# Optimization experiments

Hardware: AMD Instinct MI355X
Metric: run time of the kernel (lower is better)

## Reference

```python
import jax, jax.numpy as jnp
import numpy as np

BIGNET_DIM = 1024
N_LAYERS = 18   # 6 blocks * 3 QLoRALinear
N_LN = 5
GROUPS = 64     # 1024 / group_size(16)
GS = 16
RANK = 32
BATCH = 16384
EPS = 1e-5


def dequant(qw, scale):
    # qw: [O, G, gs] int 0..15, scale: [O, G] per-group max-abs norm
    w = (qw.astype(jnp.float32) / 15.0 * 2.0 - 1.0) * scale[..., None]
    return w.reshape(qw.shape[0], -1)  # [O, I]


def qlora_linear(x, qw, scale, b, a_w, b_w):
    w = dequant(qw, scale)                      # [O, I]
    base = x @ w.T + b                          # [N, O]
    lora = (x @ a_w.T) @ b_w.T                  # [N, r] @ [r, O]
    return base + lora


def layernorm(h, g, b):
    mu = h.mean(-1, keepdims=True)
    var = jnp.mean((h - mu) ** 2, -1, keepdims=True)
    return (h - mu) * jax.lax.rsqrt(var + EPS) * g + b


def setup_inputs() -> dict:
    key = jax.random.key(0)
    ks = jax.random.split(key, 8)
    x = jax.random.normal(ks[0], (BATCH, BIGNET_DIM), jnp.float32)
    qw = jax.random.randint(ks[1], (N_LAYERS, BIGNET_DIM, GROUPS, GS), 0, 16, jnp.int32)
    scale = jax.random.uniform(ks[2], (N_LAYERS, BIGNET_DIM, GROUPS), jnp.float32) * 0.05
    bias = jax.random.normal(ks[3], (N_LAYERS, BIGNET_DIM), jnp.float32) * 0.02
    la = jax.random.normal(ks[4], (N_LAYERS, RANK, BIGNET_DIM), jnp.float32) * (2.0 / BIGNET_DIM) ** 0.5
    # note: torch zero-inits lora_b; use small random values so the LoRA path is testable
    lb = jax.random.normal(ks[5], (N_LAYERS, BIGNET_DIM, RANK), jnp.float32) * 0.01
    ln_w = jnp.ones((N_LN, BIGNET_DIM), jnp.float32)
    ln_b = jnp.zeros((N_LN, BIGNET_DIM), jnp.float32)
    return {"x": x, "scale": scale, "bias": bias, "la": la, "lb": lb,
            "ln_w": ln_w, "ln_b": ln_b, "qw": qw}


def reference(x, scale, bias, la, lb, ln_w, ln_b, qw):
    h = x
    li = 0
    for blk in range(6):
        r = h
        for j in range(3):
            h = qlora_linear(h, qw[li], scale[li], bias[li], la[li], lb[li])
            li += 1
            if j < 2:
                h = jax.nn.relu(h)
        h = h + r
        if blk < 5:
            h = layernorm(h, ln_w[blk], ln_b[blk])
    return h
```

## Files before the change

### kernel.cpp

```cpp
#include <hip/hip_runtime.h>

typedef unsigned short UST;
typedef __attribute__((ext_vector_type(8))) __bf16 bf16x8;
typedef __attribute__((ext_vector_type(4))) float f32x4;

__device__ __forceinline__ float bf2f(UST u) {
    union { unsigned int i; float f; } v; v.i = ((unsigned int)u) << 16; return v.f;
}
__device__ __forceinline__ UST f2bf(float f) {
    union { float f; unsigned int i; } v; v.f = f;
    return (UST)((v.i + 0x7fffu + ((v.i >> 16) & 1u)) >> 16);
}

__device__ __forceinline__ void gl2lds16(const UST* g, UST* l) {
    __builtin_amdgcn_global_load_lds(
        (const __attribute__((address_space(1))) unsigned int*)g,
        (__attribute__((address_space(3))) unsigned int*)l, 16, 0, 0);
}

__global__ __launch_bounds__(256) void prep_w(
    const int* __restrict__ qw, const float* __restrict__ scale,
    const float* __restrict__ la, const float* __restrict__ lb,
    UST* __restrict__ wp)
{
    int l = blockIdx.x, ot = blockIdx.y, it = blockIdx.z;
    __shared__ float la_s[32 * 128];
    __shared__ float lb_s[128 * 32];
    const float* laL = la + (size_t)l * 32 * 1024;
    const float* lbL = lb + (size_t)l * 1024 * 32;
    int t = threadIdx.x;
    for (int e = t; e < 32 * 128; e += 256) {
        int r = e >> 7, i = e & 127;
        la_s[e] = laL[r * 1024 + it * 128 + i];
    }
    for (int e = t; e < 128 * 32; e += 256)
        lb_s[e] = lbL[(size_t)ot * 128 * 32 + e];
    __syncthreads();

    int o0 = (t >> 4) * 8;
    int i0 = (t & 15) * 8;
    float acc[8][8];
    #pragma unroll
    for (int a = 0; a < 8; a++)
        #pragma unroll
        for (int c = 0; c < 8; c++) acc[a][c] = 0.f;
    for (int r = 0; r < 32; ++r) {
        float bv[8], av[8];
        #pragma unroll
        for (int j = 0; j < 8; j++) bv[j] = lb_s[(o0 + j) * 32 + r];
        #pragma unroll
        for (int j = 0; j < 8; j++) av[j] = la_s[r * 128 + i0 + j];
        #pragma unroll
        for (int a = 0; a < 8; a++)
            #pragma unroll
            for (int c = 0; c < 8; c++) acc[a][c] += bv[a] * av[c];
    }

    const int* qL = qw + (size_t)l * 1024 * 1024;
    const float* sL = scale + (size_t)l * 1024 * 64;
    UST* wL = wp + (size_t)l * 1024 * 1024;
    #pragma unroll
    for (int a = 0; a < 8; a++) {
        int go = ot * 128 + o0 + a;
        int gi = it * 128 + i0;
        float s = sL[go * 64 + (gi >> 4)];
        UST o8[8];
        #pragma unroll
        for (int c = 0; c < 8; c++) {
            int q = qL[(size_t)go * 1024 + gi + c];
            float w = ((float)q * (2.0f / 15.0f) - 1.0f) * s + acc[a][c];
            o8[c] = f2bf(w);
        }
        *(ushort4*)(wL + (size_t)go * 1024 + gi) = make_ushort4(o8[0], o8[1], o8[2], o8[3]);
        *(ushort4*)(wL + (size_t)go * 1024 + gi + 4) = make_ushort4(o8[4], o8[5], o8[6], o8[7]);
    }
}

__global__ __launch_bounds__(256) void f32_to_bf16(const float* __restrict__ x,
                                                   UST* __restrict__ o)
{
    size_t i = ((size_t)blockIdx.x * 256 + threadIdx.x) * 4;
    float4 v = *(const float4*)(x + i);
    *(ushort4*)(o + i) = make_ushort4(f2bf(v.x), f2bf(v.y), f2bf(v.z), f2bf(v.w));
}

#define BM 128
#define BN 128
#define BK 32

__global__ __launch_bounds__(256, 4) void gemm_ep(
    const UST* __restrict__ X, const UST* __restrict__ W,
    const float* __restrict__ bias,
    UST* __restrict__ outb, const UST* __restrict__ resid,
    float* __restrict__ outf, int mode)
{
    const int K = 1024;
    __shared__ UST smem[16384];
    int tid = threadIdx.x;
    int wave = tid >> 6, lane = tid & 63;
    int wm = wave >> 1, wn = wave & 1;
    int bm = blockIdx.x, bn = blockIdx.y;
    int la15 = lane & 15, qa = lane >> 4;

    int c0 = tid, c1 = tid + 256;
    int r0 = c0 >> 2, k0c = ((c0 & 3) ^ ((r0 >> 1) & 3)) * 8;
    int r1 = c1 >> 2, k1c = ((c1 & 3) ^ ((r1 >> 1) & 3)) * 8;
    const UST* gA0 = X + (size_t)(bm * BM + r0) * K + k0c;
    const UST* gA1 = X + (size_t)(bm * BM + r1) * K + k1c;
    const UST* gB0 = W + (size_t)(bn * BN + r0) * K + k0c;
    const UST* gB1 = W + (size_t)(bn * BN + r1) * K + k1c;

    int offA[4], offB[4];
    #pragma unroll
    for (int i = 0; i < 4; i++) {
        int ra = wm * 64 + i * 16 + la15;
        offA[i] = ra * 32 + ((qa ^ ((ra >> 1) & 3)) * 8);
        int rb = wn * 64 + i * 16 + la15;
        offB[i] = rb * 32 + ((qa ^ ((rb >> 1) & 3)) * 8);
    }

    f32x4 acc[4][4];
    #pragma unroll
    for (int i = 0; i < 4; i++)
        #pragma unroll
        for (int j = 0; j < 4; j++) acc[i][j] = (f32x4){0.f, 0.f, 0.f, 0.f};

    auto issue = [&](int kk, int buf) {
        UST* dA = smem + buf * 8192;
        UST* dB = dA + 4096;
        gl2lds16(gA0 + kk, dA + c0 * 8);
        gl2lds16(gA1 + kk, dA + c1 * 8);
        gl2lds16(gB0 + kk, dB + c0 * 8);
        gl2lds16(gB1 + kk, dB + c1 * 8);
    };
    auto compute = [&](int buf) {
        const UST* pA = smem + buf * 8192;
        const UST* pB = pA + 4096;
        bf16x8 af[4], bfr[4];
        #pragma unroll
        for (int mi = 0; mi < 4; mi++) af[mi] = *(const bf16x8*)&pA[offA[mi]];
        #pragma unroll
        for (int ni = 0; ni < 4; ni++) bfr[ni] = *(const bf16x8*)&pB[offB[ni]];
        #pragma unroll
        for (int mi = 0; mi < 4; mi++)
            #pragma unroll
            for (int ni = 0; ni < 4; ni++)
                acc[mi][ni] = __builtin_amdgcn_mfma_f32_16x16x32_bf16(
                    af[mi], bfr[ni], acc[mi][ni], 0, 0, 0);
    };

    issue(0, 0);
    #pragma unroll 2
    for (int it = 0; it < 31; ++it) {
        int cur = it & 1;
        issue((it + 1) * BK, cur ^ 1);
        asm volatile("s_waitcnt vmcnt(4)\n\ts_barrier" ::: "memory");
        compute(cur);
        asm volatile("s_waitcnt lgkmcnt(0)\n\ts_barrier" ::: "memory");
    }
    asm volatile("s_waitcnt vmcnt(0)\n\ts_barrier" ::: "memory");
    compute(1);
    asm volatile("s_waitcnt lgkmcnt(0)\n\ts_barrier" ::: "memory");

    float* cs = (float*)smem;
    int cc = tid & 15, rw = tid >> 4;
    int gcolb = bn * BN + cc * 8;
    float4 bv0 = *(const float4*)&bias[gcolb];
    float4 bv1 = *(const float4*)&bias[gcolb + 4];

    #pragma unroll
    for (int h = 0; h < 2; ++h) {
        if (wm == h) {
            #pragma unroll
            for (int mi = 0; mi < 4; mi++)
                #pragma unroll
                for (int ni = 0; ni < 4; ni++) {
                    int colx = (wn * 64 + ni * 16 + la15) ^ (qa << 4);
                    #pragma unroll
                    for (int r2 = 0; r2 < 4; r2++) {
                        int rl = mi * 16 + qa * 4 + r2;
                        cs[rl * 128 + colx] = acc[mi][ni][r2];
                    }
                }
        }
        asm volatile("s_waitcnt lgkmcnt(0)\n\ts_barrier" ::: "memory");
        #pragma unroll
        for (int g = 0; g < 4; ++g) {
            int rl = g * 16 + rw;
            int swz = ((rl >> 2) & 3) << 2;
            int gr0 = ((cc * 2) ^ swz) * 4;
            float4 v0 = *(const float4*)&cs[rl * 128 + gr0];
            float4 v1 = *(const float4*)&cs[rl * 128 + gr0 + 4];
            float o0 = v0.x + bv0.x, o1 = v0.y + bv0.y;
            float o2 = v0.z + bv0.z, o3 = v0.w + bv0.w;
            float o4 = v1.x + bv1.x, o5 = v1.y + bv1.y;
            float o6 = v1.z + bv1.z, o7 = v1.w + bv1.w;
            if (mode == 0) {
                o0 = fmaxf(o0, 0.f); o1 = fmaxf(o1, 0.f);
                o2 = fmaxf(o2, 0.f); o3 = fmaxf(o3, 0.f);
                o4 = fmaxf(o4, 0.f); o5 = fmaxf(o5, 0.f);
                o6 = fmaxf(o6, 0.f); o7 = fmaxf(o7, 0.f);
            }
            int grow = bm * BM + h * 64 + rl;
            size_t base = (size_t)grow * 1024 + gcolb;
            if (mode == 2) {
                ushort4 rv0 = *(const ushort4*)&resid[base];
                ushort4 rv1 = *(const ushort4*)&resid[base + 4];
                o0 += bf2f(rv0.x); o1 += bf2f(rv0.y);
                o2 += bf2f(rv0.z); o3 += bf2f(rv0.w);
                o4 += bf2f(rv1.x); o5 += bf2f(rv1.y);
                o6 += bf2f(rv1.z); o7 += bf2f(rv1.w);
                *(float4*)&outf[base] = make_float4(o0, o1, o2, o3);
                *(float4*)&outf[base + 4] = make_float4(o4, o5, o6, o7);
            } else {
                uint4 pk;
                pk.x = (unsigned)f2bf(o0) | ((unsigned)f2bf(o1) << 16);
                pk.y = (unsigned)f2bf(o2) | ((unsigned)f2bf(o3) << 16);
                pk.z = (unsigned)f2bf(o4) | ((unsigned)f2bf(o5) << 16);
                pk.w = (unsigned)f2bf(o6) | ((unsigned)f2bf(o7) << 16);
                *(uint4*)&outb[base] = pk;
            }
        }
        asm volatile("s_waitcnt lgkmcnt(0)\n\ts_barrier" ::: "memory");
    }
}

__global__ __launch_bounds__(256) void ln_res(
    const UST* __restrict__ h3, UST* __restrict__ r,
    const float* __restrict__ g, const float* __restrict__ b)
{
    int row = blockIdx.x;
    int t = threadIdx.x;
    int lane = t & 63, wave = t >> 6;
    const ushort4* hp = (const ushort4*)(h3 + (size_t)row * 1024);
    ushort4* rp = (ushort4*)(r + (size_t)row * 1024);
    ushort4 hv = hp[t], rv = rp[t];
    float u0 = bf2f(hv.x) + bf2f(rv.x);
    float u1 = bf2f(hv.y) + bf2f(rv.y);
    float u2 = bf2f(hv.z) + bf2f(rv.z);
    float u3 = bf2f(hv.w) + bf2f(rv.w);

    float s = u0 + u1 + u2 + u3;
    #pragma unroll
    for (int off = 32; off > 0; off >>= 1) s += __shfl_down(s, off, 64);
    __shared__ float red[8];
    if (lane == 0) red[wave] = s;
    __syncthreads();
    float mean = (red[0] + red[1] + red[2] + red[3]) * (1.0f / 1024.0f);

    float d0 = u0 - mean, d1 = u1 - mean, d2 = u2 - mean, d3 = u3 - mean;
    float vs = d0 * d0 + d1 * d1 + d2 * d2 + d3 * d3;
    #pragma unroll
    for (int off = 32; off > 0; off >>= 1) vs += __shfl_down(vs, off, 64);
    if (lane == 0) red[4 + wave] = vs;
    __syncthreads();
    float var = (red[4] + red[5] + red[6] + red[7]) * (1.0f / 1024.0f);
    float rstd = rsqrtf(var + 1e-5f);

    int i0 = t * 4;
    ushort4 o;
    o.x = f2bf(d0 * rstd * g[i0 + 0] + b[i0 + 0]);
    o.y = f2bf(d1 * rstd * g[i0 + 1] + b[i0 + 1]);
    o.z = f2bf(d2 * rstd * g[i0 + 2] + b[i0 + 2]);
    o.w = f2bf(d3 * rstd * g[i0 + 3] + b[i0 + 3]);
    rp[t] = o;
}

extern "C" void kernel_launch(void* const* d_in, const int* in_sizes, int n_in,
                              void* d_out, int out_size, void* d_ws, size_t ws_size,
                              hipStream_t stream) {
    const float* x     = (const float*)d_in[0];
    const float* scale = (const float*)d_in[1];
    const float* bias  = (const float*)d_in[2];
    const float* la    = (const float*)d_in[3];
    const float* lb    = (const float*)d_in[4];
    const float* ln_w  = (const float*)d_in[5];
    const float* ln_b  = (const float*)d_in[6];
    const int*   qw    = (const int*)d_in[7];

    const int M = in_sizes[0] / 1024;
    const size_t WPB = (size_t)18 * 1024 * 1024 * 2;
    const size_t ACT = (size_t)M * 1024 * 2;

    UST* wp = (UST*)d_ws;
    UST* A  = (UST*)((char*)d_ws + WPB);
    UST* Cb = (UST*)((char*)d_ws + WPB + ACT);
    UST* Bb = (UST*)d_out;

    prep_w<<<dim3(18, 8, 8), 256, 0, stream>>>(qw, scale, la, lb, wp);
    f32_to_bf16<<<(M * 1024) / (256 * 4), 256, 0, stream>>>(x, A);

    int li = 0;
    for (int blk = 0; blk < 6; ++blk) {
        gemm_ep<<<dim3(M / 128, 8), 256, 0, stream>>>(
            A, wp + (size_t)li * 1024 * 1024, bias + li * 1024, Bb, nullptr, nullptr, 0);
        li++;
        gemm_ep<<<dim3(M / 128, 8), 256, 0, stream>>>(
            Bb, wp + (size_t)li * 1024 * 1024, bias + li * 1024, Cb, nullptr, nullptr, 0);
        li++;
        if (blk < 5) {
            gemm_ep<<<dim3(M / 128, 8), 256, 0, stream>>>(
                Cb, wp + (size_t)li * 1024 * 1024, bias + li * 1024, Bb, nullptr, nullptr, 1);
            li++;
            ln_res<<<M, 256, 0, stream>>>(Bb, A, ln_w + blk * 1024, ln_b + blk * 1024);
        } else {
            gemm_ep<<<dim3(M / 128, 8), 256, 0, stream>>>(
                Cb, wp + (size_t)li * 1024 * 1024, bias + li * 1024, nullptr, A,
                (float*)d_out, 2);
            li++;
        }
    }
}
```

Baseline: 1.117 ms.

## Triple-buffer GEMM K loop, swap grid order, and vectorize prep_w loads

```diff
diff --git a/kernel.cpp b/kernel.cpp
--- a/kernel.cpp
+++ b/kernel.cpp
@@ -25,20 +25,38 @@
 {
     int l = blockIdx.x, ot = blockIdx.y, it = blockIdx.z;
     __shared__ float la_s[32 * 128];
-    __shared__ float lb_s[128 * 32];
+    __shared__ float lb_s[128 * 33];
+    int t = threadIdx.x;
+    int o0 = (t >> 4) * 8;
+    int i0 = (t & 15) * 8;
+
+    const int* qL = qw + (size_t)l * 1024 * 1024;
+    const float* sL = scale + (size_t)l * 1024 * 64;
+
+    const int* qbase = qL + (size_t)(ot * 128 + o0) * 1024 + it * 128 + i0;
+    int4 qv[16];
+    #pragma unroll
+    for (int a = 0; a < 8; a++) {
+        qv[2 * a]     = *(const int4*)(qbase + (size_t)a * 1024);
+        qv[2 * a + 1] = *(const int4*)(qbase + (size_t)a * 1024 + 4);
+    }
+    float sc[8];
+    #pragma unroll
+    for (int a = 0; a < 8; a++)
+        sc[a] = sL[(size_t)(ot * 128 + o0 + a) * 64 + ((it * 128 + i0) >> 4)];
+
     const float* laL = la + (size_t)l * 32 * 1024;
-    const float* lbL = lb + (size_t)l * 1024 * 32;
-    int t = threadIdx.x;
+    const float* lbL = lb + (size_t)l * 1024 * 32 + (size_t)ot * 128 * 32;
     for (int e = t; e < 32 * 128; e += 256) {
         int r = e >> 7, i = e & 127;
         la_s[e] = laL[r * 1024 + it * 128 + i];
     }
-    for (int e = t; e < 128 * 32; e += 256)
-        lb_s[e] = lbL[(size_t)ot * 128 * 32 + e];
+    for (int e = t; e < 128 * 32; e += 256) {
+        int o = e >> 5, r = e & 31;
+        lb_s[o * 33 + r] = lbL[e];
+    }
     __syncthreads();
 
-    int o0 = (t >> 4) * 8;
-    int i0 = (t & 15) * 8;
     float acc[8][8];
     #pragma unroll
     for (int a = 0; a < 8; a++)
@@ -47,7 +65,7 @@
     for (int r = 0; r < 32; ++r) {
         float bv[8], av[8];
         #pragma unroll
-        for (int j = 0; j < 8; j++) bv[j] = lb_s[(o0 + j) * 32 + r];
+        for (int j = 0; j < 8; j++) bv[j] = lb_s[(o0 + j) * 33 + r];
         #pragma unroll
         for (int j = 0; j < 8; j++) av[j] = la_s[r * 128 + i0 + j];
         #pragma unroll
@@ -56,19 +74,19 @@
             for (int c = 0; c < 8; c++) acc[a][c] += bv[a] * av[c];
     }
 
-    const int* qL = qw + (size_t)l * 1024 * 1024;
-    const float* sL = scale + (size_t)l * 1024 * 64;
     UST* wL = wp + (size_t)l * 1024 * 1024;
     #pragma unroll
     for (int a = 0; a < 8; a++) {
         int go = ot * 128 + o0 + a;
         int gi = it * 128 + i0;
-        float s = sL[go * 64 + (gi >> 4)];
+        float s = sc[a];
+        int q[8];
+        q[0] = qv[2 * a].x; q[1] = qv[2 * a].y; q[2] = qv[2 * a].z; q[3] = qv[2 * a].w;
+        q[4] = qv[2 * a + 1].x; q[5] = qv[2 * a + 1].y; q[6] = qv[2 * a + 1].z; q[7] = qv[2 * a + 1].w;
         UST o8[8];
         #pragma unroll
         for (int c = 0; c < 8; c++) {
-            int q = qL[(size_t)go * 1024 + gi + c];
-            float w = ((float)q * (2.0f / 15.0f) - 1.0f) * s + acc[a][c];
+            float w = ((float)q[c] * (2.0f / 15.0f) - 1.0f) * s + acc[a][c];
             o8[c] = f2bf(w);
         }
         *(ushort4*)(wL + (size_t)go * 1024 + gi) = make_ushort4(o8[0], o8[1], o8[2], o8[3]);
@@ -88,18 +106,23 @@
 #define BN 128
 #define BK 32
 
-__global__ __launch_bounds__(256, 4) void gemm_ep(
+#define WB8 asm volatile("s_waitcnt vmcnt(8)\n\ts_barrier" ::: "memory")
+#define WB4 asm volatile("s_waitcnt vmcnt(4)\n\ts_barrier" ::: "memory")
+#define WB0 asm volatile("s_waitcnt vmcnt(0)\n\ts_barrier" ::: "memory")
+#define LGB asm volatile("s_waitcnt lgkmcnt(0)\n\ts_barrier" ::: "memory")
+
+__global__ __launch_bounds__(256, 3) void gemm_ep(
     const UST* __restrict__ X, const UST* __restrict__ W,
     const float* __restrict__ bias,
     UST* __restrict__ outb, const UST* __restrict__ resid,
     float* __restrict__ outf, int mode)
 {
     const int K = 1024;
-    __shared__ UST smem[16384];
+    __shared__ UST smem[24576];
     int tid = threadIdx.x;
     int wave = tid >> 6, lane = tid & 63;
     int wm = wave >> 1, wn = wave & 1;
-    int bm = blockIdx.x, bn = blockIdx.y;
+    int bn = blockIdx.x, bm = blockIdx.y;
     int la15 = lane & 15, qa = lane >> 4;
 
     int c0 = tid, c1 = tid + 256;
@@ -150,17 +173,15 @@
     };
 
     issue(0, 0);
-    #pragma unroll 2
-    for (int it = 0; it < 31; ++it) {
-        int cur = it & 1;
-        issue((it + 1) * BK, cur ^ 1);
-        asm volatile("s_waitcnt vmcnt(4)\n\ts_barrier" ::: "memory");
-        compute(cur);
-        asm volatile("s_waitcnt lgkmcnt(0)\n\ts_barrier" ::: "memory");
-    }
-    asm volatile("s_waitcnt vmcnt(0)\n\ts_barrier" ::: "memory");
-    compute(1);
-    asm volatile("s_waitcnt lgkmcnt(0)\n\ts_barrier" ::: "memory");
+    issue(BK, 1);
+    #pragma unroll 1
+    for (int t = 0; t < 30; t += 3) {
+        issue((t + 2) * BK, 2); WB8; compute(0); LGB;
+        issue((t + 3) * BK, 0); WB8; compute(1); LGB;
+        issue((t + 4) * BK, 1); WB8; compute(2); LGB;
+    }
+    WB4; compute(0); LGB;
+    WB0; compute(1); LGB;
 
     float* cs = (float*)smem;
     int cc = tid & 15, rw = tid >> 4;
@@ -183,7 +204,7 @@
                     }
                 }
         }
-        asm volatile("s_waitcnt lgkmcnt(0)\n\ts_barrier" ::: "memory");
+        LGB;
         #pragma unroll
         for (int g = 0; g < 4; ++g) {
             int rl = g * 16 + rw;
@@ -221,7 +242,7 @@
                 *(uint4*)&outb[base] = pk;
             }
         }
-        asm volatile("s_waitcnt lgkmcnt(0)\n\ts_barrier" ::: "memory");
+        LGB;
     }
 }
 
@@ -292,19 +313,19 @@
 
     int li = 0;
     for (int blk = 0; blk < 6; ++blk) {
-        gemm_ep<<<dim3(M / 128, 8), 256, 0, stream>>>(
+        gemm_ep<<<dim3(8, M / 128), 256, 0, stream>>>(
             A, wp + (size_t)li * 1024 * 1024, bias + li * 1024, Bb, nullptr, nullptr, 0);
         li++;
-        gemm_ep<<<dim3(M / 128, 8), 256, 0, stream>>>(
+        gemm_ep<<<dim3(8, M / 128), 256, 0, stream>>>(
             Bb, wp + (size_t)li * 1024 * 1024, bias + li * 1024, Cb, nullptr, nullptr, 0);
         li++;
         if (blk < 5) {
-            gemm_ep<<<dim3(M / 128, 8), 256, 0, stream>>>(
+            gemm_ep<<<dim3(8, M / 128), 256, 0, stream>>>(
                 Cb, wp + (size_t)li * 1024 * 1024, bias + li * 1024, Bb, nullptr, nullptr, 1);
             li++;
             ln_res<<<M, 256, 0, stream>>>(Bb, A, ln_w + blk * 1024, ln_b + blk * 1024);
         } else {
-            gemm_ep<<<dim3(M / 128, 8), 256, 0, stream>>>(
+            gemm_ep<<<dim3(8, M / 128), 256, 0, stream>>>(
                 Cb, wp + (size_t)li * 1024 * 1024, bias + li * 1024, nullptr, A,
                 (float*)d_out, 2);
             li++;
```

Measured after the change: 1.200 ms. 7.5% more time.
